# Optimization experiments

Hardware: AMD Instinct MI355X
Metric: run time of the kernel (lower is better)

The kernel has to match this reference:

```python
import jax, jax.numpy as jnp
import numpy as np

B, S, T = 64, 128, 64
V, E, H, L = 32000, 512, 512, 2
PAD, BOS = 0, 1


def setup_inputs() -> dict:
    key = jax.random.key(0)
    ks = jax.random.split(key, 14)
    w = lambda k, shape: (jax.random.normal(k, shape, jnp.float32) * 0.05)
    src_emb = w(ks[0], (V, E)).at[PAD].set(0.0)
    tgt_emb = w(ks[1], (V, E)).at[PAD].set(0.0)
    enc_Wih = w(ks[2], (L, 4 * H, E))
    enc_Whh = w(ks[3], (L, 4 * H, H))
    enc_b = w(ks[4], (L, 4 * H))          # b_ih + b_hh fused
    dec_Wih = w(ks[5], (L, 4 * H, E))
    dec_Whh = w(ks[6], (L, 4 * H, H))
    dec_b = w(ks[7], (L, 4 * H))
    gen_W = w(ks[8], (V, H))
    gen_b = jnp.zeros((V,), jnp.float32)
    x_seqs = jax.random.randint(ks[9], (B, S), 0, V, jnp.int32)
    x_len = jnp.sort(jax.random.randint(ks[10], (B,), 1, S + 1, jnp.int32))[::-1]
    y_seqs = jax.random.randint(ks[11], (B, T), 0, V, jnp.int32)
    teacher = jax.random.randint(ks[12], (T - 1,), 0, 2, jnp.int32)
    return dict(x_seqs=x_seqs, x_len=x_len, y_seqs=y_seqs, teacher=teacher,
                src_emb=src_emb, tgt_emb=tgt_emb,
                enc_Wih=enc_Wih, enc_Whh=enc_Whh, enc_b=enc_b,
                dec_Wih=dec_Wih, dec_Whh=dec_Whh, dec_b=dec_b,
                gen_W=gen_W, gen_b=gen_b)


def lstm_cell(x, h, c, Wih, Whh, b):
    # torch gate order: i, f, g, o
    g = x @ Wih.T + h @ Whh.T + b
    i, f, gg, o = jnp.split(g, 4, axis=-1)
    c2 = jax.nn.sigmoid(f) * c + jax.nn.sigmoid(i) * jnp.tanh(gg)
    h2 = jax.nn.sigmoid(o) * jnp.tanh(c2)
    return h2, c2


def encode(x_seqs, x_len, src_emb, Wih, Whh, b):
    emb = src_emb[x_seqs]                                  # [B,S,E]
    mask = jnp.arange(S)[None, :] < x_len[:, None]         # [B,S] valid steps
    inp = emb.transpose(1, 0, 2)                           # [S,B,E]
    m_t = mask.T                                           # [S,B]
    hs, cs = [], []
    for l in range(L):
        def step(carry, xs, l=l):
            h, c = carry
            xt, m = xs
            h2, c2 = lstm_cell(xt, h, c, Wih[l], Whh[l], b[l])
            m = m[:, None]
            h2 = jnp.where(m, h2, h)   # freeze state past sequence length
            c2 = jnp.where(m, c2, c)
            return (h2, c2), h2
        z = jnp.zeros((B, H), inp.dtype)
        (hT, cT), out = jax.lax.scan(step, (z, z), (inp, m_t))
        inp = out
        hs.append(hT)
        cs.append(cT)
    return jnp.stack(hs), jnp.stack(cs)                    # each [L,B,H]


def reference(x_seqs, x_len, y_seqs, teacher, src_emb, tgt_emb,
              enc_Wih, enc_Whh, enc_b, dec_Wih, dec_Whh, dec_b, gen_W, gen_b):
    h0, c0 = encode(x_seqs, x_len, src_emb, enc_Wih, enc_Whh, enc_b)

    def step(carry, xs):
        h, c, inp = carry                                  # [L,B,H],[L,B,H],[B]
        y_t, tf = xs                                       # [B], scalar flag
        x = tgt_emb[inp]                                   # [B,E]
        new_h, new_c = [], []
        for l in range(L):
            hl, cl = lstm_cell(x, h[l], c[l], dec_Wih[l], dec_Whh[l], dec_b[l])
            new_h.append(hl); new_c.append(cl)
            x = hl
        logp = jax.nn.log_softmax(x @ gen_W.T + gen_b, axis=-1)   # [B,V]
        expct = jnp.take_along_axis(logp, y_t[:, None], axis=1)[:, 0]
        pred = jnp.argmax(logp, axis=1).astype(inp.dtype)
        nxt = jnp.where(tf > 0, y_t, pred)                 # scheduled sampling
        return (jnp.stack(new_h), jnp.stack(new_c), nxt), expct

    inp0 = jnp.full((B,), BOS, jnp.int32)
    _, outp = jax.lax.scan(step, (h0, c0, inp0), (y_seqs[:, 1:].T, teacher))
    return outp.T                                          # [B, T-1]
```

## Files before the change

kernel.cpp:

```cpp
#include <hip/hip_runtime.h>
#include <hip/hip_bf16.h>
#include <cstdint>
#include <cstddef>

namespace {

constexpr int B = 64, S = 128, T = 64, V = 32000, E = 512, H = 512;
constexpr int G4 = 2048;
constexpr int TM1 = T - 1;
constexpr int CHUNK = 32;
constexpr int BH = B * H;
constexpr int NT = 128;
constexpr int NTILES = V / NT;
constexpr float MARGIN = 0.02f;
constexpr unsigned NBLK = 256;

typedef __attribute__((ext_vector_type(8))) short short8v;
typedef __attribute__((ext_vector_type(4))) float f32x4;

struct GemmSh { float As[16][68]; float Bs[16][132]; };
struct StepSh { float gs[64][17]; };
struct GenSh  { float lds[64][NT + 4]; float pv1[64][4], pv2[64][4], psum[64][4], mrow[64];
                int pi1[64][4], pi2[64][4]; };
struct RedSh  { float sM[256], sS[256], red[256]; float cV[16], rV[16]; int cI[16]; int cN, nxt; };

__device__ __forceinline__ float sigf(float x) { return 1.0f / (1.0f + expf(-x)); }

__device__ __forceinline__ void split3(float w, __hip_bfloat16& a, __hip_bfloat16& b,
                                       __hip_bfloat16& c2) {
    a = __float2bfloat16(w);
    float r = w - __bfloat162float(a);
    b = __float2bfloat16(r);
    c2 = __float2bfloat16(r - __bfloat162float(b));
}


__device__ __forceinline__ unsigned ld_coh_u32(const unsigned* p) {
    unsigned v;
    asm volatile("global_load_dword %0, %1, off sc0 sc1\n\ts_waitcnt vmcnt(0)"
                 : "=v"(v) : "v"(p) : "memory");
    return v;
}
__device__ __forceinline__ void st_coh_u32(unsigned* p, unsigned v) {
    asm volatile("global_store_dword %0, %1, off sc0 sc1" :: "v"(p), "v"(v) : "memory");
}
__device__ __forceinline__ float ld_coh_f32(const float* p) {
    float v;
    asm volatile("global_load_dword %0, %1, off sc0 sc1\n\ts_waitcnt vmcnt(0)"
                 : "=v"(v) : "v"(p));
    return v;
}
__device__ __forceinline__ void st_coh_f32(float* p, float v) {
    asm volatile("global_store_dword %0, %1, off sc0 sc1" :: "v"(p), "v"(v));
}
__device__ __forceinline__ f32x4 ld_coh_f32x4(const float* p) {
    f32x4 v;
    asm volatile("global_load_dwordx4 %0, %1, off sc0 sc1\n\ts_waitcnt vmcnt(0)"
                 : "=v"(v) : "v"(p));
    return v;
}
__device__ __forceinline__ void st_coh_b16(__hip_bfloat16* p, __hip_bfloat16 v) {
    unsigned short us; __builtin_memcpy(&us, &v, 2);
    unsigned u = us;
    asm volatile("global_store_short %0, %1, off sc0 sc1" :: "v"(p), "v"(u));
}
__device__ __forceinline__ void st_coh_b128(__hip_bfloat16* p, short8v v) {
    asm volatile("global_store_dwordx4 %0, %1, off sc0 sc1" :: "v"(p), "v"(v));
}
__device__ __forceinline__ void fence_vm() {
    asm volatile("s_waitcnt vmcnt(0)" ::: "memory");
}

__device__ __forceinline__ void ldg12(const __hip_bfloat16* p0, const __hip_bfloat16* p1,
                                      const __hip_bfloat16* p2, short8v* q)
{
    asm volatile(
        "global_load_dwordx4 %0, %12, off sc0 sc1\n\t"
        "global_load_dwordx4 %1, %12, off offset:64 sc0 sc1\n\t"
        "global_load_dwordx4 %2, %12, off offset:128 sc0 sc1\n\t"
        "global_load_dwordx4 %3, %12, off offset:192 sc0 sc1\n\t"
        "global_load_dwordx4 %4, %13, off sc0 sc1\n\t"
        "global_load_dwordx4 %5, %13, off offset:64 sc0 sc1\n\t"
        "global_load_dwordx4 %6, %13, off offset:128 sc0 sc1\n\t"
        "global_load_dwordx4 %7, %13, off offset:192 sc0 sc1\n\t"
        "global_load_dwordx4 %8, %14, off sc0 sc1\n\t"
        "global_load_dwordx4 %9, %14, off offset:64 sc0 sc1\n\t"
        "global_load_dwordx4 %10, %14, off offset:128 sc0 sc1\n\t"
        "global_load_dwordx4 %11, %14, off offset:192 sc0 sc1\n\t"
        "s_waitcnt vmcnt(0)"
        : "=&v"(q[0]), "=&v"(q[1]), "=&v"(q[2]), "=&v"(q[3]),
          "=&v"(q[4]), "=&v"(q[5]), "=&v"(q[6]), "=&v"(q[7]),
          "=&v"(q[8]), "=&v"(q[9]), "=&v"(q[10]), "=&v"(q[11])
        : "v"(p0), "v"(p1), "v"(p2));
}

__device__ __forceinline__ void ldg16(const __hip_bfloat16* p0, const __hip_bfloat16* p1,
                                      const __hip_bfloat16* p2, const __hip_bfloat16* p3,
                                      short8v* q)
{
    asm volatile(
        "global_load_dwordx4 %0, %16, off sc0 sc1\n\t"
        "global_load_dwordx4 %1, %16, off offset:64 sc0 sc1\n\t"
        "global_load_dwordx4 %2, %16, off offset:128 sc0 sc1\n\t"
        "global_load_dwordx4 %3, %16, off offset:192 sc0 sc1\n\t"
        "global_load_dwordx4 %4, %17, off sc0 sc1\n\t"
        "global_load_dwordx4 %5, %17, off offset:64 sc0 sc1\n\t"
        "global_load_dwordx4 %6, %17, off offset:128 sc0 sc1\n\t"
        "global_load_dwordx4 %7, %17, off offset:192 sc0 sc1\n\t"
        "global_load_dwordx4 %8, %18, off sc0 sc1\n\t"
        "global_load_dwordx4 %9, %18, off offset:64 sc0 sc1\n\t"
        "global_load_dwordx4 %10, %18, off offset:128 sc0 sc1\n\t"
        "global_load_dwordx4 %11, %18, off offset:192 sc0 sc1\n\t"
        "global_load_dwordx4 %12, %19, off sc0 sc1\n\t"
        "global_load_dwordx4 %13, %19, off offset:64 sc0 sc1\n\t"
        "global_load_dwordx4 %14, %19, off offset:128 sc0 sc1\n\t"
        "global_load_dwordx4 %15, %19, off offset:192 sc0 sc1\n\t"
        "s_waitcnt vmcnt(0)"
        : "=&v"(q[0]), "=&v"(q[1]), "=&v"(q[2]), "=&v"(q[3]),
          "=&v"(q[4]), "=&v"(q[5]), "=&v"(q[6]), "=&v"(q[7]),
          "=&v"(q[8]), "=&v"(q[9]), "=&v"(q[10]), "=&v"(q[11]),
          "=&v"(q[12]), "=&v"(q[13]), "=&v"(q[14]), "=&v"(q[15])
        : "v"(p0), "v"(p1), "v"(p2), "v"(p3));
}

__device__ __forceinline__ void ldg8(const __hip_bfloat16* p0, const __hip_bfloat16* p1,
                                     short8v* q)
{
    asm volatile(
        "global_load_dwordx4 %0, %8, off sc0 sc1\n\t"
        "global_load_dwordx4 %1, %8, off offset:64 sc0 sc1\n\t"
        "global_load_dwordx4 %2, %8, off offset:128 sc0 sc1\n\t"
        "global_load_dwordx4 %3, %8, off offset:192 sc0 sc1\n\t"
        "global_load_dwordx4 %4, %9, off sc0 sc1\n\t"
        "global_load_dwordx4 %5, %9, off offset:64 sc0 sc1\n\t"
        "global_load_dwordx4 %6, %9, off offset:128 sc0 sc1\n\t"
        "global_load_dwordx4 %7, %9, off offset:192 sc0 sc1\n\t"
        "s_waitcnt vmcnt(0)"
        : "=&v"(q[0]), "=&v"(q[1]), "=&v"(q[2]), "=&v"(q[3]),
          "=&v"(q[4]), "=&v"(q[5]), "=&v"(q[6]), "=&v"(q[7])
        : "v"(p0), "v"(p1));
}

__device__ __forceinline__ void gbar(unsigned* flags, unsigned* rel, unsigned& ep)
{
    unsigned tgt = ++ep;
    fence_vm();
    __syncthreads();
    const int tid = threadIdx.x;
    if (blockIdx.x == 0) {
        if (tid > 0) {
            int spins = 0;
            while (ld_coh_u32(&flags[tid * 32]) < tgt) {
                if (spins < 8) __builtin_amdgcn_s_sleep(1);
                else           __builtin_amdgcn_s_sleep(32);
                if (++spins > (1 << 16)) break;
            }
        }
        __syncthreads();
        st_coh_u32(&rel[tid * 32], tgt);
    } else {
        if (tid == 0) {
            st_coh_u32(&flags[blockIdx.x * 32], tgt);
            int spins = 0;
            while (ld_coh_u32(&rel[blockIdx.x * 32]) < tgt) {
                if (spins < 8) __builtin_amdgcn_s_sleep(1);
                else           __builtin_amdgcn_s_sleep(32);
                if (++spins > (1 << 16)) break;
            }
        }
        __syncthreads();
    }
}

__global__ __launch_bounds__(256)
void split_dec_k(const float* __restrict__ Wih, const float* __restrict__ Whh,
                 const float* __restrict__ bsrc,
                 __hip_bfloat16* __restrict__ P0, __hip_bfloat16* __restrict__ P1,
                 __hip_bfloat16* __restrict__ P2, float* __restrict__ bint)
{
    int row = blockIdx.x;
    int l = row >> 11, jp = row & 2047;
    int kh = jp >> 2, g = jp & 3, src = g * 512 + kh;
    const float* wih = Wih + ((size_t)l * 2048 + src) * 512;
    const float* whh = Whh + ((size_t)l * 2048 + src) * 512;
    size_t ro = (size_t)row * 1024;
    for (int k = threadIdx.x; k < 1024; k += 256) {
        float w = (k < 512) ? whh[k] : wih[k - 512];
        __hip_bfloat16 a, b, c2; split3(w, a, b, c2);
        P0[ro + k] = a; P1[ro + k] = b; P2[ro + k] = c2;
    }
    if (threadIdx.x == 0) bint[row] = bsrc[l * 2048 + src];
}

__global__ __launch_bounds__(256)
void split_enc_k(const float* __restrict__ Whh,
                 __hip_bfloat16* __restrict__ P0, __hip_bfloat16* __restrict__ P1,
                 __hip_bfloat16* __restrict__ P2)
{
    int row = blockIdx.x;
    int kh = row >> 2, g = row & 3, src = g * 512 + kh;
    const float* whh = Whh + (size_t)src * 512;
    size_t ro = (size_t)row * 512;
    for (int k = threadIdx.x; k < 512; k += 256) {
        __hip_bfloat16 a, b, c2; split3(whh[k], a, b, c2);
        P0[ro + k] = a; P1[ro + k] = b; P2[ro + k] = c2;
    }
}

__device__ void gemm_tile(char* shraw, const float* __restrict__ A,
                          const float* __restrict__ Wt, const float* __restrict__ bias,
                          float* __restrict__ C,
                          const int* __restrict__ xseq, int m0, int bx, int by)
{
    GemmSh* sh = reinterpret_cast<GemmSh*>(shraw);
    constexpr int K = 512, BK = 16;
    int tid = threadIdx.x;
    int bm = by * 64, bn = bx * 128;
    int tx = tid & 15, ty = tid >> 4;
    float acc[4][8] = {};

    int lm = tid >> 2, lk = (tid & 3) << 2;
    const float* Arow;
    {
        int mg = m0 + bm + lm; int tt = mg >> 6, b = mg & 63;
        Arow = A + (size_t)xseq[b * S + tt] * K;
    }
    int ln = tid >> 1, lkb = (tid & 1) << 3;
    const float* Brow = Wt + (size_t)(bn + ln) * K;

    for (int k0 = 0; k0 < K; k0 += BK) {
        float4 av = *(const float4*)(Arow + k0 + lk);
        sh->As[lk + 0][lm] = av.x; sh->As[lk + 1][lm] = av.y;
        sh->As[lk + 2][lm] = av.z; sh->As[lk + 3][lm] = av.w;
        float4 bv0 = *(const float4*)(Brow + k0 + lkb);
        float4 bv1 = *(const float4*)(Brow + k0 + lkb + 4);
        sh->Bs[lkb + 0][ln] = bv0.x; sh->Bs[lkb + 1][ln] = bv0.y;
        sh->Bs[lkb + 2][ln] = bv0.z; sh->Bs[lkb + 3][ln] = bv0.w;
        sh->Bs[lkb + 4][ln] = bv1.x; sh->Bs[lkb + 5][ln] = bv1.y;
        sh->Bs[lkb + 6][ln] = bv1.z; sh->Bs[lkb + 7][ln] = bv1.w;
        __syncthreads();
#pragma unroll
        for (int kk = 0; kk < BK; ++kk) {
            const float4 a4  = *(const float4*)&sh->As[kk][ty * 4];
            const float4 b4a = *(const float4*)&sh->Bs[kk][tx * 8];
            const float4 b4b = *(const float4*)&sh->Bs[kk][tx * 8 + 4];
            const float a[4]  = {a4.x, a4.y, a4.z, a4.w};
            const float bb[8] = {b4a.x, b4a.y, b4a.z, b4a.w,
                                 b4b.x, b4b.y, b4b.z, b4b.w};
#pragma unroll
            for (int i = 0; i < 4; ++i)
#pragma unroll
                for (int j = 0; j < 8; ++j)
                    acc[i][j] = fmaf(a[i], bb[j], acc[i][j]);
        }
        __syncthreads();
    }
#pragma unroll
    for (int i = 0; i < 4; ++i) {
        size_t crow = (size_t)(bm + ty * 4 + i) * G4;
#pragma unroll
        for (int j = 0; j < 8; ++j) {
            int cg = bn + tx * 8 + j;
            int jp = ((cg & 511) << 2) | (cg >> 9);
            st_coh_f32(C + crow + jp, acc[i][j] + bias[cg]);
        }
    }
}

template<int KHALF, bool ADDXC, bool MASK>
__device__ void step_body(char* shraw, int blk,
    const __hip_bfloat16* __restrict__ hA0, const __hip_bfloat16* __restrict__ hA1,
    const __hip_bfloat16* __restrict__ hA2,
    const __hip_bfloat16* __restrict__ xA0, const __hip_bfloat16* __restrict__ xA1,
    const __hip_bfloat16* __restrict__ xA2,
    const __hip_bfloat16* __restrict__ W0, const __hip_bfloat16* __restrict__ W1,
    const __hip_bfloat16* __restrict__ W2,
    const float* __restrict__ addsrc, const float* __restrict__ h_in,
    float* __restrict__ h_out, float* __restrict__ c,
    __hip_bfloat16* __restrict__ o0, __hip_bfloat16* __restrict__ o1,
    __hip_bfloat16* __restrict__ o2,
    const int* __restrict__ x_len, int t)
{
    StepSh* sh = reinterpret_cast<StepSh*>(shraw);
    int tid = threadIdx.x;
    int wave = tid >> 6, lane = tid & 63;
    int lr = lane & 15, kg = (lane >> 4) * 8;
    int arow = wave * 16 + lr;
    int brow = blk * 16 + lr;
    const int KW = 512 * KHALF;

    f32x4 acc0 = {0,0,0,0}, acc1 = {0,0,0,0}, acc2 = {0,0,0,0};
    const size_t aoff = (size_t)arow * 512 + kg;
    const size_t boff = (size_t)brow * KW + kg;

#pragma unroll
    for (int g = 0; g < KHALF * 4; ++g) {
        const __hip_bfloat16 *A0, *A1, *A2; size_t go;
        if (KHALF == 2 && g >= 4) { A0 = xA0; A1 = xA1; A2 = xA2;
                                    go = aoff + (size_t)(g - 4) * 128; }
        else                      { A0 = hA0; A1 = hA1; A2 = hA2;
                                    go = aoff + (size_t)g * 128; }
        short8v q[12];
        ldg12(A0 + go, A1 + go, A2 + go, q);
#pragma unroll
        for (int j = 0; j < 4; ++j) {
            int k0 = g * 128 + j * 32;
            short8v b0 = *(const short8v*)(W0 + boff + k0);
            short8v b1 = *(const short8v*)(W1 + boff + k0);
            short8v b2 = *(const short8v*)(W2 + boff + k0);
            short8v a0 = q[j], a1 = q[4 + j], a2 = q[8 + j];
            acc0 = __builtin_amdgcn_mfma_f32_16x16x32_bf16(a0, b0, acc0, 0, 0, 0);
            acc1 = __builtin_amdgcn_mfma_f32_16x16x32_bf16(a0, b1, acc1, 0, 0, 0);
            acc2 = __builtin_amdgcn_mfma_f32_16x16x32_bf16(a1, b0, acc2, 0, 0, 0);
            acc0 = __builtin_amdgcn_mfma_f32_16x16x32_bf16(a1, b1, acc0, 0, 0, 0);
            acc1 = __builtin_amdgcn_mfma_f32_16x16x32_bf16(a0, b2, acc1, 0, 0, 0);
            acc2 = __builtin_amdgcn_mfma_f32_16x16x32_bf16(a2, b0, acc2, 0, 0, 0);
        }
    }
    int rb = (lane >> 4) * 4;
#pragma unroll
    for (int r = 0; r < 4; ++r)
        sh->gs[wave * 16 + rb + r][lr] = acc0[r] + acc1[r] + acc2[r];
    __syncthreads();

    int b = tid >> 2, khl = tid & 3;
    int khg = blk * 4 + khl;
    f32x4 add;
    if (ADDXC) add = ld_coh_f32x4(addsrc + (size_t)b * G4 + (size_t)khg * 4);
    else       add = *(const f32x4*)(addsrc + (size_t)khg * 4);
    float gi = sh->gs[b][khl * 4 + 0] + add[0];
    float gf = sh->gs[b][khl * 4 + 1] + add[1];
    float gg = sh->gs[b][khl * 4 + 2] + add[2];
    float go2 = sh->gs[b][khl * 4 + 3] + add[3];
    size_t idx = (size_t)b * H + khg;
    float cold = ld_coh_f32(c + idx);
    float c2 = sigf(gf) * cold + sigf(gi) * tanhf(gg);
    float h2 = sigf(go2) * tanhf(c2);
    if (MASK) {
        bool mk = t < x_len[b];
        if (!mk) { h2 = ld_coh_f32(h_in + idx); c2 = cold; }
    }
    if (h_out) st_coh_f32(h_out + idx, h2);
    st_coh_f32(c + idx, c2);
    __hip_bfloat16 s0, s1, s2; split3(h2, s0, s1, s2);
    st_coh_b16(o0 + idx, s0); st_coh_b16(o1 + idx, s1); st_coh_b16(o2 + idx, s2);
}

__device__ void gen_body(char* shraw, int bid,
                         const __hip_bfloat16* __restrict__ hbf,
                         const __hip_bfloat16* __restrict__ Wbf,
                         const float* __restrict__ genb,
                         float* __restrict__ part)
{
    GenSh* sh = reinterpret_cast<GenSh*>(shraw);
    int tid = threadIdx.x;
    int wave = tid >> 6, lane = tid & 63;
    int n0 = bid * NT;
    int lr = lane & 15;
    int kg = (lane >> 4) * 8;

    f32x4 acc[4][2];
    const f32x4 zero = {0.f, 0.f, 0.f, 0.f};
#pragma unroll
    for (int i = 0; i < 4; ++i)
#pragma unroll
        for (int j = 0; j < 2; ++j) acc[i][j] = zero;

    const __hip_bfloat16* Arow = hbf + (size_t)lr * 512 + kg;
    const __hip_bfloat16* Brow = Wbf + (size_t)(n0 + wave * 32 + lr) * 512 + kg;
#pragma unroll
    for (int g = 0; g < 4; ++g) {
        short8v qa[16], qb[8];
        ldg16(Arow + g * 128, Arow + 8192 + g * 128,
              Arow + 16384 + g * 128, Arow + 24576 + g * 128, qa);
        ldg8(Brow + g * 128, Brow + 8192 + g * 128, qb);
#pragma unroll
        for (int j = 0; j < 4; ++j) {
#pragma unroll
            for (int mf = 0; mf < 4; ++mf)
#pragma unroll
                for (int nf = 0; nf < 2; ++nf)
                    acc[mf][nf] = __builtin_amdgcn_mfma_f32_16x16x32_bf16(
                        qa[mf * 4 + j], qb[nf * 4 + j], acc[mf][nf], 0, 0, 0);
        }
    }
#pragma unroll
    for (int nf = 0; nf < 2; ++nf) {
        int colLocal = wave * 32 + nf * 16 + lr;
        float bias = genb[n0 + colLocal];
#pragma unroll
        for (int mf = 0; mf < 4; ++mf) {
#pragma unroll
            for (int r = 0; r < 4; ++r) {
                int row = mf * 16 + (lane >> 4) * 4 + r;
                sh->lds[row][colLocal] = acc[mf][nf][r] + bias;
            }
        }
    }
    __syncthreads();

    int row = tid >> 2, q = tid & 3;
    int cbase = q * 32;
    float v1 = -3.4e38f, v2 = -3.4e38f; int i1 = 0x7fffffff, i2 = 0x7fffffff;
    for (int c = 0; c < 32; ++c) {
        float v = sh->lds[row][cbase + c];
        int ci = cbase + c;
        if (v > v1 || (v == v1 && ci < i1)) { v2 = v1; i2 = i1; v1 = v; i1 = ci; }
        else if (v > v2 || (v == v2 && ci < i2)) { v2 = v; i2 = ci; }
    }
    sh->pv1[row][q] = v1; sh->pi1[row][q] = i1; sh->pv2[row][q] = v2; sh->pi2[row][q] = i2;
    __syncthreads();

    float t1 = -3.4e38f, t2 = -3.4e38f; int j1 = 0x7fffffff, j2 = 0x7fffffff;
    if (q == 0) {
        for (int k = 0; k < 4; ++k) {
            float a1 = sh->pv1[row][k]; int a1i = sh->pi1[row][k];
            float a2 = sh->pv2[row][k]; int a2i = sh->pi2[row][k];
            if (a1 > t1 || (a1 == t1 && a1i < j1)) { t2 = t1; j2 = j1; t1 = a1; j1 = a1i; }
            else if (a1 > t2 || (a1 == t2 && a1i < j2)) { t2 = a1; j2 = a1i; }
            if (a2 > t1 || (a2 == t1 && a2i < j1)) { t2 = t1; j2 = j1; t1 = a2; j1 = a2i; }
            else if (a2 > t2 || (a2 == t2 && a2i < j2)) { t2 = a2; j2 = a2i; }
        }
        sh->mrow[row] = t1;
    }
    __syncthreads();
    float m = sh->mrow[row];
    float s = 0.f;
    for (int c = 0; c < 32; ++c) s += expf(sh->lds[row][cbase + c] - m);
    sh->psum[row][q] = s;
    __syncthreads();
    if (q == 0) {
        float sum = sh->psum[row][0] + sh->psum[row][1] + sh->psum[row][2] + sh->psum[row][3];
        float* p = part + ((size_t)bid * B + row) * 6;
        st_coh_f32(p + 0, t1);
        st_coh_f32(p + 1, t2);
        st_coh_u32((unsigned*)(p + 2), (unsigned)(n0 + j1));
        st_coh_u32((unsigned*)(p + 3), (unsigned)(n0 + j2));
        st_coh_f32(p + 4, sum);
    }
}

__device__ void reduce_body(char* shraw, int b,
                            const float* __restrict__ part,
                            const float* __restrict__ h,
                            const float* __restrict__ genW, const float* __restrict__ genb,
                            const float* __restrict__ tgt_emb,
                            const int* __restrict__ y_seqs, const int* __restrict__ teacher,
                            float* __restrict__ outp,
                            __hip_bfloat16* __restrict__ xp0, __hip_bfloat16* __restrict__ xp1,
                            __hip_bfloat16* __restrict__ xp2, int t)
{
    RedSh* sh = reinterpret_cast<RedSh*>(shraw);
    int tid = threadIdx.x;
    int y = y_seqs[b * T + t + 1];
    const float* hrow = h + (size_t)b * 512;
    float h_a = ld_coh_f32(hrow + tid);
    float h_b = ld_coh_f32(hrow + tid + 256);

    float p_top1 = -3.4e38f, p_top2 = -3.4e38f, p_sum = 0.f;
    int p_i1 = 0x7fffffff, p_i2 = 0x7fffffff;
    if (tid < NTILES) {
        const float* p = part + ((size_t)tid * B + b) * 6;
        f32x4 v4 = ld_coh_f32x4(p);
        p_top1 = v4[0]; p_top2 = v4[1];
        p_i1 = __float_as_int(v4[2]);
        p_i2 = __float_as_int(v4[3]);
        p_sum = ld_coh_f32(p + 4);
    }
    sh->sM[tid] = p_top1; __syncthreads();
    for (int o = 128; o; o >>= 1) { if (tid < o) sh->sM[tid] = fmaxf(sh->sM[tid], sh->sM[tid + o]); __syncthreads(); }
    float M = sh->sM[0];
    if (tid == 0) sh->cN = 0;
    __syncthreads();

    float Ssum = (tid < NTILES) ? p_sum * expf(p_top1 - M) : 0.f;
    if (tid < NTILES) {
        if (p_top1 >= M - MARGIN) { int j = atomicAdd(&sh->cN, 1); if (j < 16) { sh->cV[j] = p_top1; sh->cI[j] = p_i1; } }
        if (p_top2 >= M - MARGIN) { int j = atomicAdd(&sh->cN, 1); if (j < 16) { sh->cV[j] = p_top2; sh->cI[j] = p_i2; } }
    }
    sh->sS[tid] = Ssum; __syncthreads();
    for (int o = 128; o; o >>= 1) { if (tid < o) sh->sS[tid] += sh->sS[tid + o]; __syncthreads(); }
    float lse = M + logf(sh->sS[0]);
    int nc = sh->cN < 16 ? sh->cN : 16;

    {
        const float* wrow = genW + (size_t)y * 512;
        float s = fmaf(h_a, wrow[tid], 0.f) + h_b * wrow[tid + 256];
        sh->red[tid] = s; __syncthreads();
        for (int o = 128; o; o >>= 1) { if (tid < o) sh->red[tid] += sh->red[tid + o]; __syncthreads(); }
        if (tid == 0) outp[b * TM1 + t] = sh->red[0] + genb[y] - lse;
        __syncthreads();
    }
    if (nc > 1) {
        for (int j = 0; j < nc; ++j) {
            const float* wrow = genW + (size_t)sh->cI[j] * 512;
            float s = fmaf(h_a, wrow[tid], 0.f) + h_b * wrow[tid + 256];
            sh->red[tid] = s; __syncthreads();
            for (int o = 128; o; o >>= 1) { if (tid < o) sh->red[tid] += sh->red[tid + o]; __syncthreads(); }
            if (tid == 0) sh->rV[j] = sh->red[0] + genb[sh->cI[j]];
            __syncthreads();
        }
    }
    if (tid == 0) {
        int winner;
        if (nc == 1) winner = sh->cI[0];
        else {
            float bv = -3.4e38f; int bi = 0x7fffffff;
            for (int j = 0; j < nc; ++j)
                if (sh->rV[j] > bv || (sh->rV[j] == bv && sh->cI[j] < bi)) { bv = sh->rV[j]; bi = sh->cI[j]; }
            winner = bi;
        }
        sh->nxt = (teacher[t] > 0) ? y : winner;
    }
    __syncthreads();
    int tok = sh->nxt;
    for (int k = tid; k < 512; k += 256) {
        float w = tgt_emb[(size_t)tok * 512 + k];
        __hip_bfloat16 s0, s1, s2; split3(w, s0, s1, s2);
        st_coh_b16(xp0 + (size_t)b * 512 + k, s0);
        st_coh_b16(xp1 + (size_t)b * 512 + k, s1);
        st_coh_b16(xp2 + (size_t)b * 512 + k, s2);
    }
}

struct Args {
    const int *x_seqs, *x_len, *y_seqs, *teacher;
    const float *src_emb, *tgt_emb, *eWih, *eb, *genW, *genb;
    float* Xc;
    const __hip_bfloat16 *eP0, *eP1, *eP2;
    const __hip_bfloat16 *e1P0, *e1P1, *e1P2;
    const float* ebint;
    const __hip_bfloat16 *dP0, *dP1, *dP2;
    const float* bint;
    float *hf32, *cbuf, *dech1;
    __hip_bfloat16 *P, *xP, *Wbf;
    float* part;
    float* outp;
    unsigned *flags, *rel;
};

__global__ __launch_bounds__(256, 1)
void persist_k(Args a)
{
    __shared__ __align__(16) char shpool[40960];
    unsigned ep = 0;
    const int bid = blockIdx.x;
    const int tid = threadIdx.x;
    const int gtid = bid * 256 + tid;
    const int GS = NBLK * 256;

    auto Pl = [&](int l, int slot, int pl) {
        return a.P + (((size_t)(l * 2 + slot)) * 3 + pl) * BH; };

    for (int i = gtid; i < BH; i += GS) {
        st_coh_f32(a.hf32 + i, 0.f); st_coh_f32(a.hf32 + 2 * BH + i, 0.f);
        st_coh_f32(a.cbuf + i, 0.f); st_coh_f32(a.cbuf + BH + i, 0.f);
    }
    {
        unsigned* p0 = (unsigned*)Pl(0, 0, 0);
        unsigned* p1 = (unsigned*)Pl(1, 0, 0);
        for (int i = gtid; i < 3 * BH / 2; i += GS) { st_coh_u32(p0 + i, 0u); st_coh_u32(p1 + i, 0u); }
    }
    gbar(a.flags, a.rel, ep);

    for (int c0 = 0; c0 < S; c0 += CHUNK) {
        for (int tile = bid; tile < 512; tile += NBLK)
            gemm_tile(shpool, a.src_emb, a.eWih, a.eb, a.Xc,
                      a.x_seqs, c0 * B, tile & 15, tile >> 4);
        gbar(a.flags, a.rel, ep);
        for (int tl = 0; tl < CHUNK; ++tl) {
            int t = c0 + tl;
            if (bid < 128) {
                step_body<1, true, true>(shpool, bid,
                    Pl(0, t & 1, 0), Pl(0, t & 1, 1), Pl(0, t & 1, 2),
                    nullptr, nullptr, nullptr,
                    a.eP0, a.eP1, a.eP2,
                    a.Xc + (size_t)tl * B * G4,
                    a.hf32 + (size_t)(t & 1) * BH, a.hf32 + (size_t)((t + 1) & 1) * BH,
                    a.cbuf,
                    Pl(0, (t + 1) & 1, 0), Pl(0, (t + 1) & 1, 1), Pl(0, (t + 1) & 1, 2),
                    a.x_len, t);
            } else if (t >= 1) {
                int u = t - 1;
                step_body<2, false, true>(shpool, bid - 128,
                    Pl(1, u & 1, 0), Pl(1, u & 1, 1), Pl(1, u & 1, 2),
                    Pl(0, t & 1, 0), Pl(0, t & 1, 1), Pl(0, t & 1, 2),
                    a.e1P0, a.e1P1, a.e1P2,
                    a.ebint,
                    a.hf32 + (size_t)(2 + (u & 1)) * BH, a.hf32 + (size_t)(2 + ((u + 1) & 1)) * BH,
                    a.cbuf + BH,
                    Pl(1, (u + 1) & 1, 0), Pl(1, (u + 1) & 1, 1), Pl(1, (u + 1) & 1, 2),
                    a.x_len, u);
            }
            gbar(a.flags, a.rel, ep);
        }
    }
    if (bid < 128) {
        int u = S - 1;
        step_body<2, false, true>(shpool, bid,
            Pl(1, u & 1, 0), Pl(1, u & 1, 1), Pl(1, u & 1, 2),
            Pl(0, (u + 1) & 1, 0), Pl(0, (u + 1) & 1, 1), Pl(0, (u + 1) & 1, 2),
            a.e1P0, a.e1P1, a.e1P2,
            a.ebint,
            a.hf32 + (size_t)(2 + (u & 1)) * BH, a.hf32 + (size_t)(2 + ((u + 1) & 1)) * BH,
            a.cbuf + BH,
            Pl(1, (u + 1) & 1, 0), Pl(1, (u + 1) & 1, 1), Pl(1, (u + 1) & 1, 2),
            a.x_len, u);
    }
    gbar(a.flags, a.rel, ep);

    {
        const int N8 = V * E / 8;
        for (int i = gtid; i < N8; i += GS) {
            float4 x = *(const float4*)(a.genW + (size_t)i * 8);
            float4 y = *(const float4*)(a.genW + (size_t)i * 8 + 4);
            __hip_bfloat16 tmp[8];
            tmp[0] = __float2bfloat16(x.x); tmp[1] = __float2bfloat16(x.y);
            tmp[2] = __float2bfloat16(x.z); tmp[3] = __float2bfloat16(x.w);
            tmp[4] = __float2bfloat16(y.x); tmp[5] = __float2bfloat16(y.y);
            tmp[6] = __float2bfloat16(y.z); tmp[7] = __float2bfloat16(y.w);
            st_coh_b128(a.Wbf + (size_t)i * 8, *(const short8v*)tmp);
        }
        for (int i = gtid; i < BH; i += GS) {
            int k = i & 511;
            float w = a.tgt_emb[512 + k];
            __hip_bfloat16 s0, s1, s2; split3(w, s0, s1, s2);
            st_coh_b16(a.xP + i, s0);
            st_coh_b16(a.xP + BH + i, s1);
            st_coh_b16(a.xP + 2 * BH + i, s2);
        }
    }
    gbar(a.flags, a.rel, ep);

    for (int t = 0; t < TM1; ++t) {
        int si = t & 1, so = si ^ 1;
        if (bid < 128)
            step_body<2, false, false>(shpool, bid,
                Pl(0, si, 0), Pl(0, si, 1), Pl(0, si, 2),
                a.xP, a.xP + BH, a.xP + 2 * BH,
                a.dP0, a.dP1, a.dP2, a.bint,
                nullptr, nullptr, a.cbuf,
                Pl(0, so, 0), Pl(0, so, 1), Pl(0, so, 2),
                nullptr, 0);
        gbar(a.flags, a.rel, ep);
        if (bid < 128)
            step_body<2, false, false>(shpool, bid,
                Pl(1, si, 0), Pl(1, si, 1), Pl(1, si, 2),
                Pl(0, so, 0), Pl(0, so, 1), Pl(0, so, 2),
                a.dP0 + (size_t)G4 * 1024, a.dP1 + (size_t)G4 * 1024,
                a.dP2 + (size_t)G4 * 1024, a.bint + G4,
                nullptr, a.dech1, a.cbuf + BH,
                Pl(1, so, 0), Pl(1, so, 1), Pl(1, so, 2),
                nullptr, 0);
        gbar(a.flags, a.rel, ep);
        if (bid < NTILES)
            gen_body(shpool, bid, Pl(1, so, 0), a.Wbf, a.genb, a.part);
        gbar(a.flags, a.rel, ep);
        if (bid < B)
            reduce_body(shpool, bid, a.part, a.dech1, a.genW, a.genb, a.tgt_emb,
                        a.y_seqs, a.teacher, a.outp,
                        a.xP, a.xP + BH, a.xP + 2 * BH, t);
        gbar(a.flags, a.rel, ep);
    }
}

}

extern "C" void kernel_launch(void* const* d_in, const int* in_sizes, int n_in,
                              void* d_out, int out_size, void* d_ws, size_t ws_size,
                              hipStream_t stream)
{
    (void)in_sizes; (void)n_in; (void)out_size;
    const int*   x_seqs  = (const int*)  d_in[0];
    const int*   x_len   = (const int*)  d_in[1];
    const int*   y_seqs  = (const int*)  d_in[2];
    const int*   teacher = (const int*)  d_in[3];
    const float* src_emb = (const float*)d_in[4];
    const float* tgt_emb = (const float*)d_in[5];
    const float* eWih    = (const float*)d_in[6];
    const float* eWhh    = (const float*)d_in[7];
    const float* eb      = (const float*)d_in[8];
    const float* dWih    = (const float*)d_in[9];
    const float* dWhh    = (const float*)d_in[10];
    const float* db      = (const float*)d_in[11];
    const float* genW    = (const float*)d_in[12];
    const float* genb    = (const float*)d_in[13];

    float* w = (float*)d_ws;
    size_t off = 0;
    auto take = [&](size_t n) { float* p = w + off; off += n; return p; };
    auto takeb = [&](size_t n) { return (__hip_bfloat16*)take((n + 1) / 2); };

    unsigned* flags = (unsigned*)take(256 * 32);
    unsigned* rel   = (unsigned*)take(256 * 32);
    float* Xc = take((size_t)CHUNK * B * G4);
    __hip_bfloat16* eP0  = takeb((size_t)G4 * 512);
    __hip_bfloat16* eP1  = takeb((size_t)G4 * 512);
    __hip_bfloat16* eP2  = takeb((size_t)G4 * 512);
    __hip_bfloat16* e1P0 = takeb((size_t)G4 * 1024);
    __hip_bfloat16* e1P1 = takeb((size_t)G4 * 1024);
    __hip_bfloat16* e1P2 = takeb((size_t)G4 * 1024);
    float* ebint = take((size_t)G4);
    __hip_bfloat16* dP0 = takeb((size_t)2 * G4 * 1024);
    __hip_bfloat16* dP1 = takeb((size_t)2 * G4 * 1024);
    __hip_bfloat16* dP2 = takeb((size_t)2 * G4 * 1024);
    float* bint  = take(2 * (size_t)G4);
    float* hf32  = take(4 * (size_t)BH);
    float* cbuf  = take(2 * (size_t)BH);
    float* dech1 = take((size_t)BH);
    __hip_bfloat16* P  = takeb((size_t)12 * BH);
    __hip_bfloat16* xP = takeb((size_t)3 * BH);
    float* part_f = take((size_t)NTILES * B * 6);
    if (ws_size < off * sizeof(float)) return;

    dim3 tpb256(256);
    split_enc_k<<<dim3(G4), tpb256, 0, stream>>>(eWhh, eP0, eP1, eP2);
    split_dec_k<<<dim3(G4), tpb256, 0, stream>>>(
        eWih + (size_t)G4 * E, eWhh + (size_t)G4 * E, eb + G4, e1P0, e1P1, e1P2, ebint);
    split_dec_k<<<dim3(2 * G4), tpb256, 0, stream>>>(
        dWih, dWhh, db, dP0, dP1, dP2, bint);
    hipError_t _e = hipMemsetAsync(flags, 0, 2 * 256 * 32 * sizeof(unsigned), stream);
    (void)_e;

    Args a;
    a.x_seqs = x_seqs; a.x_len = x_len; a.y_seqs = y_seqs; a.teacher = teacher;
    a.src_emb = src_emb; a.tgt_emb = tgt_emb; a.eWih = eWih; a.eb = eb;
    a.genW = genW; a.genb = genb;
    a.Xc = Xc;
    a.eP0 = eP0; a.eP1 = eP1; a.eP2 = eP2;
    a.e1P0 = e1P0; a.e1P1 = e1P1; a.e1P2 = e1P2; a.ebint = ebint;
    a.dP0 = dP0; a.dP1 = dP1; a.dP2 = dP2; a.bint = bint;
    a.hf32 = hf32; a.cbuf = cbuf; a.dech1 = dech1;
    a.P = P; a.xP = xP;
    a.Wbf = (__hip_bfloat16*)Xc;
    a.part = part_f;
    a.outp = (float*)d_out;
    a.flags = flags; a.rel = rel;

    persist_k<<<dim3(NBLK), tpb256, 0, stream>>>(a);
}
```

Measured before the change: 10.36 ms.

## Widen LSTM step tiles to 64 gate columns per block, using 32 blocks

Each recurrent step block now computes four 16-column MFMA tiles (64 gate rows, 16 hidden units) instead of one, so each loaded A fragment of h/x is reused across four weight tiles. Only 32 blocks per layer do step work, down from 128. The epilogue writes c, h and the bf16 split planes with vectorized 4-wide stores. The aim is less redundant activation loading and fewer, wider coherent stores, at the cost of less parallelism per step and more accumulator registers per thread.

```diff
diff --git a/kernel.cpp b/kernel.cpp
--- a/kernel.cpp
+++ b/kernel.cpp
@@ -17,9 +17,10 @@
 
 typedef __attribute__((ext_vector_type(8))) short short8v;
 typedef __attribute__((ext_vector_type(4))) float f32x4;
+typedef __attribute__((ext_vector_type(2))) unsigned u32x2;
 
 struct GemmSh { float As[16][68]; float Bs[16][132]; };
-struct StepSh { float gs[64][17]; };
+struct StepSh { float gs[64][68]; };
 struct GenSh  { float lds[64][NT + 4]; float pv1[64][4], pv2[64][4], psum[64][4], mrow[64];
                 int pi1[64][4], pi2[64][4]; };
 struct RedSh  { float sM[256], sS[256], red[256]; float cV[16], rV[16]; int cI[16]; int cN, nxt; };
@@ -33,6 +34,9 @@
     b = __float2bfloat16(r);
     c2 = __float2bfloat16(r - __bfloat162float(b));
 }
+__device__ __forceinline__ unsigned short bf16bits(__hip_bfloat16 v) {
+    unsigned short u; __builtin_memcpy(&u, &v, 2); return u;
+}
 
 
 __device__ __forceinline__ unsigned ld_coh_u32(const unsigned* p) {
@@ -59,10 +63,16 @@
                  : "=v"(v) : "v"(p));
     return v;
 }
+__device__ __forceinline__ void st_coh_f32x4(float* p, f32x4 v) {
+    asm volatile("global_store_dwordx4 %0, %1, off sc0 sc1" :: "v"(p), "v"(v));
+}
 __device__ __forceinline__ void st_coh_b16(__hip_bfloat16* p, __hip_bfloat16 v) {
     unsigned short us; __builtin_memcpy(&us, &v, 2);
     unsigned u = us;
     asm volatile("global_store_short %0, %1, off sc0 sc1" :: "v"(p), "v"(u));
+}
+__device__ __forceinline__ void st_coh_b64(__hip_bfloat16* p, u32x2 v) {
+    asm volatile("global_store_dwordx2 %0, %1, off sc0 sc1" :: "v"(p), "v"(v));
 }
 __device__ __forceinline__ void st_coh_b128(__hip_bfloat16* p, short8v v) {
     asm volatile("global_store_dwordx4 %0, %1, off sc0 sc1" :: "v"(p), "v"(v));
@@ -286,12 +296,19 @@
     int wave = tid >> 6, lane = tid & 63;
     int lr = lane & 15, kg = (lane >> 4) * 8;
     int arow = wave * 16 + lr;
-    int brow = blk * 16 + lr;
     const int KW = 512 * KHALF;
-
-    f32x4 acc0 = {0,0,0,0}, acc1 = {0,0,0,0}, acc2 = {0,0,0,0};
     const size_t aoff = (size_t)arow * 512 + kg;
-    const size_t boff = (size_t)brow * KW + kg;
+    size_t boff[4];
+#pragma unroll
+    for (int ct = 0; ct < 4; ++ct)
+        boff[ct] = (size_t)(blk * 64 + ct * 16 + lr) * KW + kg;
+
+    f32x4 acc[4][3];
+    const f32x4 zero = {0.f, 0.f, 0.f, 0.f};
+#pragma unroll
+    for (int ct = 0; ct < 4; ++ct)
+#pragma unroll
+        for (int p = 0; p < 3; ++p) acc[ct][p] = zero;
 
 #pragma unroll
     for (int g = 0; g < KHALF * 4; ++g) {
@@ -300,50 +317,76 @@
                                     go = aoff + (size_t)(g - 4) * 128; }
         else                      { A0 = hA0; A1 = hA1; A2 = hA2;
                                     go = aoff + (size_t)g * 128; }
-        short8v q[12];
-        ldg12(A0 + go, A1 + go, A2 + go, q);
+        short8v qa[12];
+        ldg12(A0 + go, A1 + go, A2 + go, qa);
 #pragma unroll
         for (int j = 0; j < 4; ++j) {
             int k0 = g * 128 + j * 32;
-            short8v b0 = *(const short8v*)(W0 + boff + k0);
-            short8v b1 = *(const short8v*)(W1 + boff + k0);
-            short8v b2 = *(const short8v*)(W2 + boff + k0);
-            short8v a0 = q[j], a1 = q[4 + j], a2 = q[8 + j];
-            acc0 = __builtin_amdgcn_mfma_f32_16x16x32_bf16(a0, b0, acc0, 0, 0, 0);
-            acc1 = __builtin_amdgcn_mfma_f32_16x16x32_bf16(a0, b1, acc1, 0, 0, 0);
-            acc2 = __builtin_amdgcn_mfma_f32_16x16x32_bf16(a1, b0, acc2, 0, 0, 0);
-            acc0 = __builtin_amdgcn_mfma_f32_16x16x32_bf16(a1, b1, acc0, 0, 0, 0);
-            acc1 = __builtin_amdgcn_mfma_f32_16x16x32_bf16(a0, b2, acc1, 0, 0, 0);
-            acc2 = __builtin_amdgcn_mfma_f32_16x16x32_bf16(a2, b0, acc2, 0, 0, 0);
+            short8v a0 = qa[j], a1 = qa[4 + j], a2 = qa[8 + j];
+#pragma unroll
+            for (int ct = 0; ct < 4; ++ct) {
+                short8v b0 = *(const short8v*)(W0 + boff[ct] + k0);
+                short8v b1 = *(const short8v*)(W1 + boff[ct] + k0);
+                short8v b2 = *(const short8v*)(W2 + boff[ct] + k0);
+                acc[ct][0] = __builtin_amdgcn_mfma_f32_16x16x32_bf16(a0, b0, acc[ct][0], 0, 0, 0);
+                acc[ct][1] = __builtin_amdgcn_mfma_f32_16x16x32_bf16(a0, b1, acc[ct][1], 0, 0, 0);
+                acc[ct][2] = __builtin_amdgcn_mfma_f32_16x16x32_bf16(a1, b0, acc[ct][2], 0, 0, 0);
+                acc[ct][0] = __builtin_amdgcn_mfma_f32_16x16x32_bf16(a1, b1, acc[ct][0], 0, 0, 0);
+                acc[ct][1] = __builtin_amdgcn_mfma_f32_16x16x32_bf16(a0, b2, acc[ct][1], 0, 0, 0);
+                acc[ct][2] = __builtin_amdgcn_mfma_f32_16x16x32_bf16(a2, b0, acc[ct][2], 0, 0, 0);
+            }
         }
     }
     int rb = (lane >> 4) * 4;
 #pragma unroll
     for (int r = 0; r < 4; ++r)
-        sh->gs[wave * 16 + rb + r][lr] = acc0[r] + acc1[r] + acc2[r];
+#pragma unroll
+        for (int ct = 0; ct < 4; ++ct)
+            sh->gs[wave * 16 + rb + r][ct * 16 + lr] =
+                acc[ct][0][r] + acc[ct][1][r] + acc[ct][2][r];
     __syncthreads();
 
-    int b = tid >> 2, khl = tid & 3;
-    int khg = blk * 4 + khl;
-    f32x4 add;
-    if (ADDXC) add = ld_coh_f32x4(addsrc + (size_t)b * G4 + (size_t)khg * 4);
-    else       add = *(const f32x4*)(addsrc + (size_t)khg * 4);
-    float gi = sh->gs[b][khl * 4 + 0] + add[0];
-    float gf = sh->gs[b][khl * 4 + 1] + add[1];
-    float gg = sh->gs[b][khl * 4 + 2] + add[2];
-    float go2 = sh->gs[b][khl * 4 + 3] + add[3];
-    size_t idx = (size_t)b * H + khg;
-    float cold = ld_coh_f32(c + idx);
-    float c2 = sigf(gf) * cold + sigf(gi) * tanhf(gg);
-    float h2 = sigf(go2) * tanhf(c2);
-    if (MASK) {
-        bool mk = t < x_len[b];
-        if (!mk) { h2 = ld_coh_f32(h_in + idx); c2 = cold; }
-    }
-    if (h_out) st_coh_f32(h_out + idx, h2);
-    st_coh_f32(c + idx, c2);
-    __hip_bfloat16 s0, s1, s2; split3(h2, s0, s1, s2);
-    st_coh_b16(o0 + idx, s0); st_coh_b16(o1 + idx, s1); st_coh_b16(o2 + idx, s2);
+    int b = tid >> 2, q = tid & 3;
+    int m0 = q * 4;
+    int khg0 = blk * 16 + m0;
+    size_t idx0 = (size_t)b * H + khg0;
+    f32x4 cold4 = ld_coh_f32x4(c + idx0);
+    f32x4 hin4 = {0.f, 0.f, 0.f, 0.f};
+    bool mk = true;
+    if (MASK) { mk = (t < x_len[b]); if (!mk) hin4 = ld_coh_f32x4(h_in + idx0); }
+    f32x4 h4, c4;
+#pragma unroll
+    for (int kk = 0; kk < 4; ++kk) {
+        int m = m0 + kk;
+        f32x4 add;
+        if (ADDXC) add = ld_coh_f32x4(addsrc + (size_t)b * G4 + (size_t)(khg0 + kk) * 4);
+        else       add = *(const f32x4*)(addsrc + (size_t)(khg0 + kk) * 4);
+        float gi  = sh->gs[b][m * 4 + 0] + add[0];
+        float gf  = sh->gs[b][m * 4 + 1] + add[1];
+        float gg  = sh->gs[b][m * 4 + 2] + add[2];
+        float go2 = sh->gs[b][m * 4 + 3] + add[3];
+        float c2 = sigf(gf) * cold4[kk] + sigf(gi) * tanhf(gg);
+        float h2 = sigf(go2) * tanhf(c2);
+        if (MASK && !mk) { h2 = hin4[kk]; c2 = cold4[kk]; }
+        h4[kk] = h2; c4[kk] = c2;
+    }
+    st_coh_f32x4(c + idx0, c4);
+    if (h_out) st_coh_f32x4(h_out + idx0, h4);
+    unsigned short s0b[4], s1b[4], s2b[4];
+#pragma unroll
+    for (int kk = 0; kk < 4; ++kk) {
+        __hip_bfloat16 s0, s1, s2; split3(h4[kk], s0, s1, s2);
+        s0b[kk] = bf16bits(s0); s1b[kk] = bf16bits(s1); s2b[kk] = bf16bits(s2);
+    }
+    u32x2 p0 = {(unsigned)s0b[0] | ((unsigned)s0b[1] << 16),
+                (unsigned)s0b[2] | ((unsigned)s0b[3] << 16)};
+    u32x2 p1 = {(unsigned)s1b[0] | ((unsigned)s1b[1] << 16),
+                (unsigned)s1b[2] | ((unsigned)s1b[3] << 16)};
+    u32x2 p2 = {(unsigned)s2b[0] | ((unsigned)s2b[1] << 16),
+                (unsigned)s2b[2] | ((unsigned)s2b[3] << 16)};
+    st_coh_b64(o0 + idx0, p0);
+    st_coh_b64(o1 + idx0, p1);
+    st_coh_b64(o2 + idx0, p2);
 }
 
 __device__ void gen_body(char* shraw, int bid,
@@ -570,7 +613,7 @@
         gbar(a.flags, a.rel, ep);
         for (int tl = 0; tl < CHUNK; ++tl) {
             int t = c0 + tl;
-            if (bid < 128) {
+            if (bid < 32) {
                 step_body<1, true, true>(shpool, bid,
                     Pl(0, t & 1, 0), Pl(0, t & 1, 1), Pl(0, t & 1, 2),
                     nullptr, nullptr, nullptr,
@@ -580,9 +623,9 @@
                     a.cbuf,
                     Pl(0, (t + 1) & 1, 0), Pl(0, (t + 1) & 1, 1), Pl(0, (t + 1) & 1, 2),
                     a.x_len, t);
-            } else if (t >= 1) {
+            } else if (bid < 64 && t >= 1) {
                 int u = t - 1;
-                step_body<2, false, true>(shpool, bid - 128,
+                step_body<2, false, true>(shpool, bid - 32,
                     Pl(1, u & 1, 0), Pl(1, u & 1, 1), Pl(1, u & 1, 2),
                     Pl(0, t & 1, 0), Pl(0, t & 1, 1), Pl(0, t & 1, 2),
                     a.e1P0, a.e1P1, a.e1P2,
@@ -595,7 +638,7 @@
             gbar(a.flags, a.rel, ep);
         }
     }
-    if (bid < 128) {
+    if (bid < 32) {
         int u = S - 1;
         step_body<2, false, true>(shpool, bid,
             Pl(1, u & 1, 0), Pl(1, u & 1, 1), Pl(1, u & 1, 2),
@@ -634,7 +677,7 @@
 
     for (int t = 0; t < TM1; ++t) {
         int si = t & 1, so = si ^ 1;
-        if (bid < 128)
+        if (bid < 32)
             step_body<2, false, false>(shpool, bid,
                 Pl(0, si, 0), Pl(0, si, 1), Pl(0, si, 2),
                 a.xP, a.xP + BH, a.xP + 2 * BH,
@@ -643,7 +686,7 @@
                 Pl(0, so, 0), Pl(0, so, 1), Pl(0, so, 2),
                 nullptr, 0);
         gbar(a.flags, a.rel, ep);
-        if (bid < 128)
+        if (bid < 32)
             step_body<2, false, false>(shpool, bid,
                 Pl(1, si, 0), Pl(1, si, 1), Pl(1, si, 2),
                 Pl(0, so, 0), Pl(0, so, 1), Pl(0, so, 2),
```

After: 20.23 ms. 1.95x slower.
